# Performance work log

Measured on AMD Instinct MI355X. Metric: run time of the kernel, lower is better.

Reference implementation:

```python
import jax, jax.numpy as jnp
import numpy as np
from math import sqrt

B, S, D, H = 2, 2048, 1024, 16
HD = D // H


def setup_inputs() -> dict:
    key = jax.random.key(0)
    ks = jax.random.split(key, 5)
    std = 0.02
    return {
        "tensor_in": jax.random.normal(ks[0], (B, S, D), dtype=jnp.float32),
        "attention_mask": jnp.zeros((1, 1, S, S), dtype=jnp.float32),
        "Wq": jax.random.normal(ks[1], (D, D), dtype=jnp.float32) * std,
        "Wk": jax.random.normal(ks[2], (D, D), dtype=jnp.float32) * std,
        "Wv": jax.random.normal(ks[3], (D, D), dtype=jnp.float32) * std,
        "Wo": jax.random.normal(ks[4], (D, D), dtype=jnp.float32) * std,
    }


def reference(tensor_in, attention_mask, Wq, Wk, Wv, Wo):
    # nn.Linear(dim, dim, bias=False): y = x @ W.T, W is [out, in]
    q = tensor_in @ Wq.T  # [B,S,D]
    k = tensor_in @ Wk.T
    v = tensor_in @ Wv.T
    # split heads -> [B,H,S,HD]
    q = q.reshape(B, S, H, HD).transpose(0, 2, 1, 3)
    k = k.reshape(B, S, H, HD).transpose(0, 2, 1, 3)
    v = v.reshape(B, S, H, HD).transpose(0, 2, 1, 3)
    # scores [B,H,S,S]; note: mask added BEFORE scaling, scale = sqrt(full dim)
    scores = jnp.einsum("bhqd,bhkd->bhqk", q, k) + attention_mask
    weights = jax.nn.softmax(scores / sqrt(D), axis=-1)  # dropout = identity (eval)
    context = jnp.einsum("bhqk,bhkd->bhqd", weights, v)
    context = context.transpose(0, 2, 1, 3).reshape(B, S, D)
    return context @ Wo.T
```

## Files before the change

kernel.cpp:

```cpp
#include <hip/hip_runtime.h>

#define B_  2
#define S_  2048
#define D_  1024
#define H_  16
#define HD_ 64
#define M_  (B_*S_)

typedef __attribute__((ext_vector_type(8))) short  short8;
typedef __attribute__((ext_vector_type(4))) float  float4v;
typedef __attribute__((ext_vector_type(4))) int    int4v;
typedef __attribute__((ext_vector_type(4))) unsigned short ushort4v;

#define PSCALE 0.0450843341f

__device__ __forceinline__ unsigned int pack2_bf16(float a, float b) {
#if __has_builtin(__builtin_amdgcn_cvt_pk_bf16_f32)
    auto p = __builtin_amdgcn_cvt_pk_bf16_f32(a, b);
    return __builtin_bit_cast(unsigned int, p);
#else
    unsigned int xa = __builtin_bit_cast(unsigned int, a);
    unsigned int xb = __builtin_bit_cast(unsigned int, b);
    xa += 0x7fffu + ((xa >> 16) & 1u);
    xb += 0x7fffu + ((xb >> 16) & 1u);
    return (xa >> 16) | (xb & 0xffff0000u);
#endif
}
__device__ __forceinline__ unsigned short f_to_bf16bits(float f) {
#if __has_builtin(__builtin_amdgcn_cvt_pk_bf16_f32)
    return (unsigned short)(pack2_bf16(f, f) & 0xffffu);
#else
    unsigned int x = __builtin_bit_cast(unsigned int, f);
    x += 0x7fffu + ((x >> 16) & 1u);
    return (unsigned short)(x >> 16);
#endif
}

__device__ __forceinline__ float fast_exp2(float x) {
#if __has_builtin(__builtin_amdgcn_exp2f)
    return __builtin_amdgcn_exp2f(x);
#else
    return exp2f(x);
#endif
}

__global__ __launch_bounds__(256) void cvt_bf16(
    const float* __restrict__ X,  const float* __restrict__ Wq,
    const float* __restrict__ Wk, const float* __restrict__ Wv,
    const float* __restrict__ Wo,
    unsigned short* __restrict__ Xb,  unsigned short* __restrict__ Wqb,
    unsigned short* __restrict__ Wkb, unsigned short* __restrict__ Wvb,
    unsigned short* __restrict__ Wob)
{
    const long t = (long)blockIdx.x * 256 + threadIdx.x;
    const long e = t * 8;
    const float* src; unsigned short* dst; long off;
    if      (e < 4194304) { src = X;  dst = Xb;  off = e; }
    else if (e < 5242880) { src = Wq; dst = Wqb; off = e - 4194304; }
    else if (e < 6291456) { src = Wk; dst = Wkb; off = e - 5242880; }
    else if (e < 7340032) { src = Wv; dst = Wvb; off = e - 6291456; }
    else                  { src = Wo; dst = Wob; off = e - 7340032; }
    float4v a = *(const float4v*)&src[off];
    float4v b = *(const float4v*)&src[off + 4];
    int4v o;
    o[0] = (int)pack2_bf16(a[0], a[1]);
    o[1] = (int)pack2_bf16(a[2], a[3]);
    o[2] = (int)pack2_bf16(b[0], b[1]);
    o[3] = (int)pack2_bf16(b[2], b[3]);
    *(int4v*)&dst[off] = o;
}

__global__ __launch_bounds__(256) void gemm_bt(
    const unsigned short* __restrict__ A,
    const unsigned short* __restrict__ B0,
    const unsigned short* __restrict__ B1,
    const unsigned short* __restrict__ B2,
    void* __restrict__ O0, void* __restrict__ O1, void* __restrict__ O2,
    int mode_base)
{
    const int K = 1024;
    const int z = blockIdx.z;
    const int mode = mode_base + z;
    const unsigned short* Aop;
    const unsigned short* Bop;
    void* Op = (z == 0) ? O0 : (z == 1) ? O1 : O2;
    int m0, n0;
    if (mode == 2) {
        Aop = B2; Bop = A;
        m0 = blockIdx.y * 128;
        n0 = blockIdx.x * 128;
    } else {
        Aop = A;
        Bop = (z == 0) ? B0 : (z == 1) ? B1 : B2;
        m0 = blockIdx.x * 128;
        n0 = blockIdx.y * 128;
    }

    __shared__ alignas(16) unsigned short As[128 * 64];
    __shared__ alignas(16) unsigned short Bs[128 * 64];

    const int tid  = threadIdx.x;
    const int wv   = tid >> 6;
    const int lane = tid & 63;
    const int wm   = wv >> 1, wn = wv & 1;
    const int q4   = lane >> 4, l15 = lane & 15;

    const unsigned short* gA[4];
    const unsigned short* gB[4];
    int ldsoff[4];
#pragma unroll
    for (int j = 0; j < 4; j++) {
        const int r = wv * 32 + j * 8 + (lane >> 3);
        const int c = (((lane & 7) ^ (r & 7)) * 8);
        gA[j] = Aop + (long)(m0 + r) * K + c;
        gB[j] = Bop + (long)(n0 + r) * K + c;
        ldsoff[j] = (wv * 32 + j * 8) * 64 + lane * 8;
    }

    int aoff[2][4], boff[2][4];
#pragma unroll
    for (int ks = 0; ks < 2; ks++)
#pragma unroll
        for (int t = 0; t < 4; t++) {
            const int swz = (((ks * 4 + q4) ^ (l15 & 7)) * 8);
            aoff[ks][t] = (wm * 64 + t * 16 + l15) * 64 + swz;
            boff[ks][t] = (wn * 64 + t * 16 + l15) * 64 + swz;
        }

    float4v acc[4][4];
#pragma unroll
    for (int i = 0; i < 4; i++)
#pragma unroll
        for (int j = 0; j < 4; j++) acc[i][j] = (float4v)0.0f;

    int4v ar[4], br[4];
#pragma unroll
    for (int j = 0; j < 4; j++) {
        ar[j] = *(const int4v*)gA[j];
        br[j] = *(const int4v*)gB[j];
        gA[j] += 64; gB[j] += 64;
    }

    for (int k0 = 0; k0 < K; k0 += 64) {
        __syncthreads();
#pragma unroll
        for (int j = 0; j < 4; j++) {
            *(int4v*)&As[ldsoff[j]] = ar[j];
            *(int4v*)&Bs[ldsoff[j]] = br[j];
        }
        __syncthreads();

        if (k0 + 64 < K) {
#pragma unroll
            for (int j = 0; j < 4; j++) {
                ar[j] = *(const int4v*)gA[j];
                br[j] = *(const int4v*)gB[j];
                gA[j] += 64; gB[j] += 64;
            }
        }

#pragma unroll
        for (int ks = 0; ks < 2; ks++) {
            short8 afr[4], bfr[4];
#pragma unroll
            for (int mt = 0; mt < 4; mt++) afr[mt] = *(const short8*)&As[aoff[ks][mt]];
#pragma unroll
            for (int nt = 0; nt < 4; nt++) bfr[nt] = *(const short8*)&Bs[boff[ks][nt]];
#pragma unroll
            for (int mt = 0; mt < 4; mt++)
#pragma unroll
                for (int nt = 0; nt < 4; nt++)
                    acc[mt][nt] = __builtin_amdgcn_mfma_f32_16x16x32_bf16(
                        afr[mt], bfr[nt], acc[mt][nt], 0, 0, 0);
        }
    }

#pragma unroll
    for (int mt = 0; mt < 4; mt++)
#pragma unroll
        for (int nt = 0; nt < 4; nt++)
#pragma unroll
            for (int r = 0; r < 4; r++) {
                const int m = m0 + wm * 64 + mt * 16 + q4 * 4 + r;
                const int n = n0 + wn * 64 + nt * 16 + l15;
                float v = acc[mt][nt][r];
                if (mode == 3) {
                    ((float*)Op)[(long)m * D_ + n] = v;
                } else if (mode == 2) {
                    const long off = (((long)(n >> 11) * H_ + (m >> 6)) * HD_ + (m & 63)) * S_ + (n & 2047);
                    ((unsigned short*)Op)[off] = f_to_bf16bits(v);
                } else {
                    const long off = ((long)((m >> 11) * H_ + (n >> 6)) * S_ + (m & 2047)) * HD_ + (n & 63);
                    if (mode == 0) v *= PSCALE;
                    ((unsigned short*)Op)[off] = f_to_bf16bits(v);
                }
            }
}

__global__ __launch_bounds__(128) void attn(
    const unsigned short* __restrict__ Q,
    const unsigned short* __restrict__ Kk,
    const unsigned short* __restrict__ Vt,
    const float* __restrict__ mask,
    unsigned short* __restrict__ ctx)
{
    __shared__ alignas(16) unsigned short Ks [64 * 72];
    __shared__ alignas(16) unsigned short Vts[64 * 72];
    __shared__ alignas(16) unsigned short Ps [2][32 * 72];

    const int tid  = threadIdx.x;
    const int wv   = tid >> 6;
    const int lane = tid & 63;
    const int q4   = lane >> 4, l15 = lane & 15;
    const int bh   = blockIdx.y;
    const int q0   = blockIdx.x * 64;

    const long head = (long)bh * S_ * HD_;

    short8 qfr[2][2];
#pragma unroll
    for (int mt = 0; mt < 2; mt++) {
        const int qrow = q0 + wv * 32 + mt * 16 + l15;
        qfr[mt][0] = *(const short8*)&Q[head + (long)qrow * HD_ + q4 * 8];
        qfr[mt][1] = *(const short8*)&Q[head + (long)qrow * HD_ + 32 + q4 * 8];
    }

    float l_acc[2][4];
#pragma unroll
    for (int mt = 0; mt < 2; mt++)
#pragma unroll
        for (int r = 0; r < 4; r++) l_acc[mt][r] = 0.0f;
    float4v oacc[2][4];
#pragma unroll
    for (int mt = 0; mt < 2; mt++)
#pragma unroll
        for (int dt = 0; dt < 4; dt++) oacc[mt][dt] = (float4v)0.0f;

    const int srow = tid >> 3;
    const int scol = (tid & 7) * 8;
    const unsigned short* gK[4];
    const unsigned short* gV[4];
    int ldsOff[4];
#pragma unroll
    for (int j = 0; j < 4; j++) {
        const int row = j * 16 + srow;
        gK[j] = Kk + head + (long)row * HD_ + scol;
        gV[j] = Vt + head + (long)row * S_  + scol;
        ldsOff[j] = row * 72 + scol;
    }

    const float* mrow[2][4];
#pragma unroll
    for (int mt = 0; mt < 2; mt++)
#pragma unroll
        for (int r = 0; r < 4; r++)
            mrow[mt][r] = mask + (long)(q0 + wv * 32 + mt * 16 + q4 * 4 + r) * S_ + l15;

    for (int k0 = 0; k0 < S_; k0 += 64) {
        __syncthreads();
#pragma unroll
        for (int j = 0; j < 4; j++) {
            *(int4v*)&Ks [ldsOff[j]] = *(const int4v*)(gK[j] + (long)k0 * HD_);
            *(int4v*)&Vts[ldsOff[j]] = *(const int4v*)(gV[j] + k0);
        }
        __syncthreads();

        float mv[2][4][4];
#pragma unroll
        for (int mt = 0; mt < 2; mt++)
#pragma unroll
            for (int nt = 0; nt < 4; nt++)
#pragma unroll
                for (int r = 0; r < 4; r++)
                    mv[mt][nt][r] = mrow[mt][r][k0 + nt * 16];

        float4v sfr[2][4];
#pragma unroll
        for (int nt = 0; nt < 4; nt++) {
            short8 kb0 = *(const short8*)&Ks[(nt * 16 + l15) * 72 + q4 * 8];
            short8 kb1 = *(const short8*)&Ks[(nt * 16 + l15) * 72 + 32 + q4 * 8];
#pragma unroll
            for (int mt = 0; mt < 2; mt++) {
                float4v s = (float4v)0.0f;
                s = __builtin_amdgcn_mfma_f32_16x16x32_bf16(qfr[mt][0], kb0, s, 0, 0, 0);
                s = __builtin_amdgcn_mfma_f32_16x16x32_bf16(qfr[mt][1], kb1, s, 0, 0, 0);
                sfr[mt][nt] = s;
            }
        }

#pragma unroll
        for (int mt = 0; mt < 2; mt++)
#pragma unroll
            for (int nt = 0; nt < 4; nt++)
#pragma unroll
                for (int r = 0; r < 4; r++) {
                    const float p = fast_exp2(fmaf(mv[mt][nt][r], PSCALE, sfr[mt][nt][r]));
                    l_acc[mt][r] += p;
                    Ps[wv][(mt * 16 + q4 * 4 + r) * 72 + nt * 16 + l15] = f_to_bf16bits(p);
                }

        short8 pf[2][2];
#pragma unroll
        for (int mt = 0; mt < 2; mt++) {
            pf[mt][0] = *(const short8*)&Ps[wv][(mt * 16 + l15) * 72 + q4 * 8];
            pf[mt][1] = *(const short8*)&Ps[wv][(mt * 16 + l15) * 72 + 32 + q4 * 8];
        }

#pragma unroll
        for (int dt = 0; dt < 4; dt++) {
            short8 vb0 = *(const short8*)&Vts[(dt * 16 + l15) * 72 + q4 * 8];
            short8 vb1 = *(const short8*)&Vts[(dt * 16 + l15) * 72 + 32 + q4 * 8];
#pragma unroll
            for (int mt = 0; mt < 2; mt++) {
                float4v o = oacc[mt][dt];
                o = __builtin_amdgcn_mfma_f32_16x16x32_bf16(pf[mt][0], vb0, o, 0, 0, 0);
                o = __builtin_amdgcn_mfma_f32_16x16x32_bf16(pf[mt][1], vb1, o, 0, 0, 0);
                oacc[mt][dt] = o;
            }
        }
    }

#pragma unroll
    for (int mt = 0; mt < 2; mt++)
#pragma unroll
        for (int r = 0; r < 4; r++) {
#pragma unroll
            for (int off = 1; off < 16; off <<= 1)
                l_acc[mt][r] += __shfl_xor(l_acc[mt][r], off);
        }

    const int b = bh >> 4, h = bh & 15;
#pragma unroll
    for (int mt = 0; mt < 2; mt++)
#pragma unroll
        for (int dt = 0; dt < 4; dt++)
#pragma unroll
            for (int r = 0; r < 4; r++) {
                const int qg = q0 + wv * 32 + mt * 16 + q4 * 4 + r;
                const int d  = dt * 16 + l15;
                const float v = oacc[mt][dt][r] / l_acc[mt][r];
                ctx[((long)(b * S_ + qg)) * D_ + h * HD_ + d] = f_to_bf16bits(v);
            }
}

extern "C" void kernel_launch(void* const* d_in, const int* in_sizes, int n_in,
                              void* d_out, int out_size, void* d_ws, size_t ws_size,
                              hipStream_t stream) {
    const float* X    = (const float*)d_in[0];
    const float* mask = (const float*)d_in[1];
    const float* Wq   = (const float*)d_in[2];
    const float* Wk   = (const float*)d_in[3];
    const float* Wv   = (const float*)d_in[4];
    const float* Wo   = (const float*)d_in[5];
    float* out        = (float*)d_out;

    unsigned short* ws = (unsigned short*)d_ws;
    unsigned short* qws  = ws;
    unsigned short* kws  = ws + 4194304;
    unsigned short* vtws = ws + 8388608;
    unsigned short* ctx  = ws + 12582912;
    unsigned short* Xb   = ws + 16777216;
    unsigned short* Wqb  = ws + 20971520;
    unsigned short* Wkb  = ws + 22020096;
    unsigned short* Wvb  = ws + 23068672;
    unsigned short* Wob  = ws + 24117248;

    cvt_bf16<<<dim3(4096), 256, 0, stream>>>(X, Wq, Wk, Wv, Wo, Xb, Wqb, Wkb, Wvb, Wob);
    gemm_bt<<<dim3(32, 8, 3), 256, 0, stream>>>(Xb, Wqb, Wkb, Wvb, qws, kws, vtws, 0);
    attn<<<dim3(32, 32, 1), 128, 0, stream>>>(qws, kws, vtws, mask, ctx);
    gemm_bt<<<dim3(32, 8, 1), 256, 0, stream>>>(ctx, Wob, Wob, Wob, out, out, out, 3);
}
```

Before: 225.6 us.

## Split attention KV range across waves, read K/V directly from global

The attention kernel changes from two waves each handling 32 query rows over the full key range to two waves sharing the same 32 query rows, each taking half the keys (split-K). The partial outputs and row sums are then combined through LDS. K and V tiles are no longer staged in shared memory; each wave loads its MFMA fragments straight from global memory, and the per-iteration __syncthreads go away. The change also adds s_setprio around the MFMA sections, raises the occupancy hint, and swaps the grid so blocks of the same head run together. The tradeoff is more global/L2 traffic for K/V with no reuse between waves, plus a reduction epilogue, in exchange for less LDS use, fewer barriers and twice as many blocks.

Measured after the change: 311.0 us. 37.8% more time.

```diff
diff --git a/kernel.cpp b/kernel.cpp
--- a/kernel.cpp
+++ b/kernel.cpp
@@ -10,7 +10,6 @@
 typedef __attribute__((ext_vector_type(8))) short  short8;
 typedef __attribute__((ext_vector_type(4))) float  float4v;
 typedef __attribute__((ext_vector_type(4))) int    int4v;
-typedef __attribute__((ext_vector_type(4))) unsigned short ushort4v;
 
 #define PSCALE 0.0450843341f
 
@@ -197,30 +196,31 @@
             }
 }
 
-__global__ __launch_bounds__(128) void attn(
+__global__ __launch_bounds__(128, 4) void attn(
     const unsigned short* __restrict__ Q,
     const unsigned short* __restrict__ Kk,
     const unsigned short* __restrict__ Vt,
     const float* __restrict__ mask,
     unsigned short* __restrict__ ctx)
 {
-    __shared__ alignas(16) unsigned short Ks [64 * 72];
-    __shared__ alignas(16) unsigned short Vts[64 * 72];
-    __shared__ alignas(16) unsigned short Ps [2][32 * 72];
+    __shared__ alignas(16) unsigned short Ps[2][32 * 72];
+    float4v* Cmb = (float4v*)&Ps[0][0];
+    float*   Lmb = (float*)((char*)&Ps[0][0] + 8192);
 
     const int tid  = threadIdx.x;
     const int wv   = tid >> 6;
     const int lane = tid & 63;
     const int q4   = lane >> 4, l15 = lane & 15;
-    const int bh   = blockIdx.y;
-    const int q0   = blockIdx.x * 64;
+    const int bh   = blockIdx.x;
+    const int q0   = blockIdx.y * 32;
 
     const long head = (long)bh * S_ * HD_;
+    const int kbase = wv * (S_ / 2);
 
     short8 qfr[2][2];
 #pragma unroll
     for (int mt = 0; mt < 2; mt++) {
-        const int qrow = q0 + wv * 32 + mt * 16 + l15;
+        const int qrow = q0 + mt * 16 + l15;
         qfr[mt][0] = *(const short8*)&Q[head + (long)qrow * HD_ + q4 * 8];
         qfr[mt][1] = *(const short8*)&Q[head + (long)qrow * HD_ + 32 + q4 * 8];
     }
@@ -236,49 +236,33 @@
 #pragma unroll
         for (int dt = 0; dt < 4; dt++) oacc[mt][dt] = (float4v)0.0f;
 
-    const int srow = tid >> 3;
-    const int scol = (tid & 7) * 8;
-    const unsigned short* gK[4];
-    const unsigned short* gV[4];
-    int ldsOff[4];
-#pragma unroll
-    for (int j = 0; j < 4; j++) {
-        const int row = j * 16 + srow;
-        gK[j] = Kk + head + (long)row * HD_ + scol;
-        gV[j] = Vt + head + (long)row * S_  + scol;
-        ldsOff[j] = row * 72 + scol;
-    }
-
     const float* mrow[2][4];
 #pragma unroll
     for (int mt = 0; mt < 2; mt++)
 #pragma unroll
         for (int r = 0; r < 4; r++)
-            mrow[mt][r] = mask + (long)(q0 + wv * 32 + mt * 16 + q4 * 4 + r) * S_ + l15;
-
-    for (int k0 = 0; k0 < S_; k0 += 64) {
-        __syncthreads();
-#pragma unroll
-        for (int j = 0; j < 4; j++) {
-            *(int4v*)&Ks [ldsOff[j]] = *(const int4v*)(gK[j] + (long)k0 * HD_);
-            *(int4v*)&Vts[ldsOff[j]] = *(const int4v*)(gV[j] + k0);
-        }
-        __syncthreads();
-
-        float mv[2][4][4];
-#pragma unroll
-        for (int mt = 0; mt < 2; mt++)
-#pragma unroll
-            for (int nt = 0; nt < 4; nt++)
-#pragma unroll
-                for (int r = 0; r < 4; r++)
-                    mv[mt][nt][r] = mrow[mt][r][k0 + nt * 16];
+            mrow[mt][r] = mask + (long)(q0 + mt * 16 + q4 * 4 + r) * S_ + l15;
+
+    const unsigned short* Kbase = Kk + head + (long)(l15)*HD_ + q4 * 8;
+    const unsigned short* Vbase = Vt + head + (long)(l15)*S_ + q4 * 8;
+
+    for (int it = 0; it < S_ / 128; it++) {
+        const int k0 = kbase + it * 64;
+
+        float mv0[4][4];
+#pragma unroll
+        for (int nt = 0; nt < 4; nt++)
+#pragma unroll
+            for (int r = 0; r < 4; r++)
+                mv0[nt][r] = mrow[0][r][k0 + nt * 16];
 
         float4v sfr[2][4];
+        __builtin_amdgcn_s_setprio(1);
 #pragma unroll
         for (int nt = 0; nt < 4; nt++) {
-            short8 kb0 = *(const short8*)&Ks[(nt * 16 + l15) * 72 + q4 * 8];
-            short8 kb1 = *(const short8*)&Ks[(nt * 16 + l15) * 72 + 32 + q4 * 8];
+            const unsigned short* kp = Kbase + (long)(k0 + nt * 16) * HD_;
+            short8 kb0 = *(const short8*)kp;
+            short8 kb1 = *(const short8*)(kp + 32);
 #pragma unroll
             for (int mt = 0; mt < 2; mt++) {
                 float4v s = (float4v)0.0f;
@@ -287,17 +271,39 @@
                 sfr[mt][nt] = s;
             }
         }
-
-#pragma unroll
-        for (int mt = 0; mt < 2; mt++)
-#pragma unroll
-            for (int nt = 0; nt < 4; nt++)
-#pragma unroll
-                for (int r = 0; r < 4; r++) {
-                    const float p = fast_exp2(fmaf(mv[mt][nt][r], PSCALE, sfr[mt][nt][r]));
-                    l_acc[mt][r] += p;
-                    Ps[wv][(mt * 16 + q4 * 4 + r) * 72 + nt * 16 + l15] = f_to_bf16bits(p);
-                }
+        __builtin_amdgcn_s_setprio(0);
+
+        float mv1[4][4];
+#pragma unroll
+        for (int nt = 0; nt < 4; nt++)
+#pragma unroll
+            for (int r = 0; r < 4; r++)
+                mv1[nt][r] = mrow[1][r][k0 + nt * 16];
+
+#pragma unroll
+        for (int nt = 0; nt < 4; nt++)
+#pragma unroll
+            for (int r = 0; r < 4; r++) {
+                const float p = fast_exp2(fmaf(mv0[nt][r], PSCALE, sfr[0][nt][r]));
+                l_acc[0][r] += p;
+                Ps[wv][(q4 * 4 + r) * 72 + nt * 16 + l15] = f_to_bf16bits(p);
+            }
+#pragma unroll
+        for (int nt = 0; nt < 4; nt++)
+#pragma unroll
+            for (int r = 0; r < 4; r++) {
+                const float p = fast_exp2(fmaf(mv1[nt][r], PSCALE, sfr[1][nt][r]));
+                l_acc[1][r] += p;
+                Ps[wv][(16 + q4 * 4 + r) * 72 + nt * 16 + l15] = f_to_bf16bits(p);
+            }
+
+        short8 vb[4][2];
+#pragma unroll
+        for (int dt = 0; dt < 4; dt++) {
+            const unsigned short* vp = Vbase + (long)(dt * 16) * S_ + k0;
+            vb[dt][0] = *(const short8*)vp;
+            vb[dt][1] = *(const short8*)(vp + 32);
+        }
 
         short8 pf[2][2];
 #pragma unroll
@@ -306,41 +312,70 @@
             pf[mt][1] = *(const short8*)&Ps[wv][(mt * 16 + l15) * 72 + 32 + q4 * 8];
         }
 
-#pragma unroll
-        for (int dt = 0; dt < 4; dt++) {
-            short8 vb0 = *(const short8*)&Vts[(dt * 16 + l15) * 72 + q4 * 8];
-            short8 vb1 = *(const short8*)&Vts[(dt * 16 + l15) * 72 + 32 + q4 * 8];
+        __builtin_amdgcn_s_setprio(1);
+#pragma unroll
+        for (int dt = 0; dt < 4; dt++)
 #pragma unroll
             for (int mt = 0; mt < 2; mt++) {
                 float4v o = oacc[mt][dt];
-                o = __builtin_amdgcn_mfma_f32_16x16x32_bf16(pf[mt][0], vb0, o, 0, 0, 0);
-                o = __builtin_amdgcn_mfma_f32_16x16x32_bf16(pf[mt][1], vb1, o, 0, 0, 0);
+                o = __builtin_amdgcn_mfma_f32_16x16x32_bf16(pf[mt][0], vb[dt][0], o, 0, 0, 0);
+                o = __builtin_amdgcn_mfma_f32_16x16x32_bf16(pf[mt][1], vb[dt][1], o, 0, 0, 0);
                 oacc[mt][dt] = o;
             }
-        }
-    }
-
-#pragma unroll
-    for (int mt = 0; mt < 2; mt++)
-#pragma unroll
-        for (int r = 0; r < 4; r++) {
-#pragma unroll
-            for (int off = 1; off < 16; off <<= 1)
-                l_acc[mt][r] += __shfl_xor(l_acc[mt][r], off);
-        }
-
-    const int b = bh >> 4, h = bh & 15;
-#pragma unroll
-    for (int mt = 0; mt < 2; mt++)
-#pragma unroll
-        for (int dt = 0; dt < 4; dt++)
+        __builtin_amdgcn_s_setprio(0);
+    }
+
+    __syncthreads();
+    if (wv == 1) {
+#pragma unroll
+        for (int mt = 0; mt < 2; mt++)
+#pragma unroll
+            for (int dt = 0; dt < 4; dt++)
+                Cmb[(mt * 4 + dt) * 64 + lane] = oacc[mt][dt];
+#pragma unroll
+        for (int mt = 0; mt < 2; mt++)
+#pragma unroll
+            for (int r = 0; r < 4; r++)
+                Lmb[(mt * 4 + r) * 64 + lane] = l_acc[mt][r];
+    }
+    __syncthreads();
+    if (wv == 0) {
+#pragma unroll
+        for (int mt = 0; mt < 2; mt++)
+#pragma unroll
+            for (int dt = 0; dt < 4; dt++) {
+                float4v t = Cmb[(mt * 4 + dt) * 64 + lane];
+                oacc[mt][dt][0] += t[0]; oacc[mt][dt][1] += t[1];
+                oacc[mt][dt][2] += t[2]; oacc[mt][dt][3] += t[3];
+            }
+#pragma unroll
+        for (int mt = 0; mt < 2; mt++)
+#pragma unroll
+            for (int r = 0; r < 4; r++)
+                l_acc[mt][r] += Lmb[(mt * 4 + r) * 64 + lane];
+
+#pragma unroll
+        for (int mt = 0; mt < 2; mt++)
 #pragma unroll
             for (int r = 0; r < 4; r++) {
-                const int qg = q0 + wv * 32 + mt * 16 + q4 * 4 + r;
-                const int d  = dt * 16 + l15;
-                const float v = oacc[mt][dt][r] / l_acc[mt][r];
-                ctx[((long)(b * S_ + qg)) * D_ + h * HD_ + d] = f_to_bf16bits(v);
-            }
+#pragma unroll
+                for (int off = 1; off < 16; off <<= 1)
+                    l_acc[mt][r] += __shfl_xor(l_acc[mt][r], off);
+            }
+
+        const int b = bh >> 4, h = bh & 15;
+#pragma unroll
+        for (int mt = 0; mt < 2; mt++)
+#pragma unroll
+            for (int dt = 0; dt < 4; dt++)
+#pragma unroll
+                for (int r = 0; r < 4; r++) {
+                    const int qg = q0 + mt * 16 + q4 * 4 + r;
+                    const int d  = dt * 16 + l15;
+                    const float v = oacc[mt][dt][r] / l_acc[mt][r];
+                    ctx[((long)(b * S_ + qg)) * D_ + h * HD_ + d] = f_to_bf16bits(v);
+                }
+    }
 }
 
 extern "C" void kernel_launch(void* const* d_in, const int* in_sizes, int n_in,
@@ -367,6 +402,6 @@
 
     cvt_bf16<<<dim3(4096), 256, 0, stream>>>(X, Wq, Wk, Wv, Wo, Xb, Wqb, Wkb, Wvb, Wob);
     gemm_bt<<<dim3(32, 8, 3), 256, 0, stream>>>(Xb, Wqb, Wkb, Wvb, qws, kws, vtws, 0);
-    attn<<<dim3(32, 32, 1), 128, 0, stream>>>(qws, kws, vtws, mask, ctx);
+    attn<<<dim3(32, 64, 1), 128, 0, stream>>>(qws, kws, vtws, mask, ctx);
     gemm_bt<<<dim3(32, 8, 1), 256, 0, stream>>>(ctx, Wob, Wob, Wob, out, out, out, 3);
 }
```
